# Optimization experiments

Hardware: AMD Instinct MI355X
Metric: run time of the kernel (lower is better)

## Reference

```python
import jax, jax.numpy as jnp
import numpy as np

B, N, H = 512, 100, 768
I = 2 * H  # intermediate_dim default = hidden_dim * 2
NUM_ANS = 16
MAX_ANS = 15
LN_EPS = 1e-5


def setup_inputs() -> dict:
    key = jax.random.key(0)
    ks = jax.random.split(key, 7)
    s = 0.02
    return {
        "v_emb": jax.random.normal(ks[0], (B, N, H), dtype=jnp.float32),
        "W1": jax.random.normal(ks[1], (H, I), dtype=jnp.float32) * s,
        "b1": jax.random.normal(ks[2], (I,), dtype=jnp.float32) * s,
        "gamma": jnp.ones((I,), dtype=jnp.float32),
        "beta": jnp.zeros((I,), dtype=jnp.float32),
        "W2": jax.random.normal(ks[3], (I, 1), dtype=jnp.float32) * s,
        "b2": jax.random.normal(ks[4], (1,), dtype=jnp.float32) * s,
    }


def reference(v_emb, W1, b1, gamma, beta, W2, b2):
    # Linear -> GELU (exact/erf, torch nn.GELU default) -> LayerNorm -> Linear
    h = jnp.einsum("bnh,hi->bni", v_emb, W1) + b1            # [B,N,I]
    h = jax.nn.gelu(h, approximate=False)
    mu = jnp.mean(h, axis=-1, keepdims=True)
    var = jnp.mean(jnp.square(h - mu), axis=-1, keepdims=True)
    h = (h - mu) * jax.lax.rsqrt(var + LN_EPS) * gamma + beta
    scores = jnp.einsum("bni,io->bno", h, W2) + b2           # [B,N,1]
    scores = jax.nn.sigmoid(scores)                           # sigmoid=True branch
    pred = jnp.sum(scores, axis=1)                            # [B,1]
    # pred_to_logits: vectorized round + clamp + one-hot scatter
    # str(int(round(p))) in {'0'..'15'} -> that id; negative -> 0; overflow -> max_ans
    aid = jnp.clip(jnp.round(pred[:, 0]).astype(jnp.int32), 0, MAX_ANS)
    logits = jax.nn.one_hot(aid, NUM_ANS, dtype=scores.dtype)  # [B,16]
    # original returns dict: scores, final_attention_map (==scores), pred, logits
    return scores, pred, logits
```

## Files before the change

### kernel.cpp

```cpp
#include <hip/hip_runtime.h>
#include <hip/hip_bf16.h>
#include <cstdint>
#include <cstddef>

#define BB   512
#define NN   100
#define HH   768
#define II   1536
#define MM   (BB*NN)

typedef __bf16 bf16;
typedef __bf16 bf16x4 __attribute__((ext_vector_type(4)));
typedef __bf16 bf16x8 __attribute__((ext_vector_type(8)));
typedef float  f32x4  __attribute__((ext_vector_type(4)));

__device__ __forceinline__ void gld_lds16(const bf16* g, bf16* l) {
    __builtin_amdgcn_global_load_lds(
        (const __attribute__((address_space(1))) void*)g,
        (__attribute__((address_space(3))) void*)l, 16, 0, 0);
}

template <int PAT>
__device__ __forceinline__ float swz_add(float x) {
    return x + __int_as_float(
        __builtin_amdgcn_ds_swizzle(__float_as_int(x), PAT));
}
__device__ __forceinline__ float red16(float x) {
    x = swz_add<0x041F>(x);
    x = swz_add<0x081F>(x);
    x = swz_add<0x101F>(x);
    x = swz_add<0x201F>(x);
    return x;
}

__device__ __forceinline__ float fast_gelu(float x) {
    const float ax = fabsf(x) * 0.70710678118654752f;
    const float t  = __builtin_amdgcn_rcpf(fmaf(0.3275911f, ax, 1.0f));
    float p = fmaf(1.061405429f, t, -1.453152027f);
    p = fmaf(p, t, 1.421413741f);
    p = fmaf(p, t, -0.284496736f);
    p = fmaf(p, t, 0.254829592f);
    p = p * t;
    const float e    = __expf(-ax * ax);
    const float erfa = fmaf(-p, e, 1.0f);
    const float erfx = copysignf(erfa, x);
    return 0.5f * x * (1.0f + erfx);
}

__global__ __launch_bounds__(256) void prep_kernel(
    const float* __restrict__ W1, const float* __restrict__ gamma,
    const float* __restrict__ beta, const float* __restrict__ W2,
    const float* __restrict__ b2,
    bf16* __restrict__ Wp, float* __restrict__ gw, float* __restrict__ scal)
{
    int bid = blockIdx.x;
    if (bid < 1152) {
        int t  = bid * 256 + threadIdx.x;
        int n  = t % II;
        int k0 = (t / II) * 4;
        bf16x4 v;
        v[0] = (bf16)W1[(size_t)(k0+0)*II + n];
        v[1] = (bf16)W1[(size_t)(k0+1)*II + n];
        v[2] = (bf16)W1[(size_t)(k0+2)*II + n];
        v[3] = (bf16)W1[(size_t)(k0+3)*II + n];
        *(bf16x4*)&Wp[(size_t)n*HH + k0] = v;
    } else if (bid == 1152) {
        for (int j = threadIdx.x; j < II; j += 256)
            gw[j] = gamma[j] * W2[j];
    } else {
        float s1 = 0.f, s2 = 0.f;
        for (int j = threadIdx.x; j < II; j += 256) {
            float w2 = W2[j];
            s1 += gamma[j] * w2;
            s2 += beta[j]  * w2;
        }
        #pragma unroll
        for (int off = 32; off; off >>= 1) {
            s1 += __shfl_down(s1, off, 64);
            s2 += __shfl_down(s2, off, 64);
        }
        __shared__ float a1[4], a2[4];
        int lane = threadIdx.x & 63, w = threadIdx.x >> 6;
        if (lane == 0) { a1[w] = s1; a2[w] = s2; }
        __syncthreads();
        if (threadIdx.x == 0) {
            scal[0] = a1[0] + a1[1] + a1[2] + a1[3];
            scal[1] = a2[0] + a2[1] + a2[2] + a2[3] + b2[0];
        }
    }
}

__global__ __launch_bounds__(256) void gemm_part(
    const float* __restrict__ Af, const bf16* __restrict__ Wp,
    const float* __restrict__ b1, const float* __restrict__ gw,
    float* __restrict__ part)
{
    __shared__ bf16  As[128 * 64];
    __shared__ bf16  Bs[128 * 64];
    __shared__ float sred[2][128][3];

    const int tid  = threadIdx.x;
    const int lin  = (blockIdx.x % 8) * 600 + blockIdx.x / 8;
    const int mb   = lin / 12;
    const int nb   = lin % 12;
    const int lane = tid & 63;
    const int w    = tid >> 6;
    const int wm   = w >> 1;
    const int wn   = w & 1;
    const int m15  = lane & 15;
    const int q    = lane >> 4;
    const int row0 = mb * 128;

    const int rsub = tid >> 3;
    const int kg   = (tid & 7) ^ (rsub & 7);
    const int lbase = tid * 8;

    const float* aP = Af + (size_t)(row0    + rsub) * HH + kg * 8;
    const bf16*  bP = Wp + (size_t)(nb*128 + rsub) * HH + kg * 8;

    f32x4 acc[4][4] = {};

    for (int kt = 0; kt < 12; ++kt) {
        #pragma unroll
        for (int it = 0; it < 4; ++it)
            gld_lds16(bP + (size_t)it * 32 * HH, &Bs[lbase + it * 2048]);
        #pragma unroll
        for (int it = 0; it < 4; ++it) {
            const float* s = aP + (size_t)it * 32 * HH;
            float4 v0 = *(const float4*)(s);
            float4 v1 = *(const float4*)(s + 4);
            bf16x8 o = { (bf16)v0.x, (bf16)v0.y, (bf16)v0.z, (bf16)v0.w,
                         (bf16)v1.x, (bf16)v1.y, (bf16)v1.z, (bf16)v1.w };
            *(bf16x8*)&As[lbase + it * 2048] = o;
        }
        asm volatile("s_waitcnt vmcnt(0)" ::: "memory");
        __syncthreads();

        #pragma unroll
        for (int kb = 0; kb < 2; ++kb) {
            const int swz = (((kb * 4 + q) ^ (m15 & 7)) * 8);
            bf16x8 af[4], bfr[4];
            #pragma unroll
            for (int mt = 0; mt < 4; ++mt)
                af[mt] = *(const bf16x8*)&As[(wm*64 + mt*16 + m15) * 64 + swz];
            #pragma unroll
            for (int nt = 0; nt < 4; ++nt)
                bfr[nt] = *(const bf16x8*)&Bs[(wn*64 + nt*16 + m15) * 64 + swz];
            #pragma unroll
            for (int mt = 0; mt < 4; ++mt)
                #pragma unroll
                for (int nt = 0; nt < 4; ++nt)
                    acc[mt][nt] = __builtin_amdgcn_mfma_f32_16x16x32_bf16(
                        af[mt], bfr[nt], acc[mt][nt], 0, 0, 0);
        }
        __syncthreads();
        aP += 64; bP += 64;
    }

    float bv[4], gv[4];
    #pragma unroll
    for (int nt = 0; nt < 4; ++nt) {
        const int col = nb*128 + wn*64 + nt*16 + m15;
        bv[nt] = b1[col];
        gv[nt] = gw[col];
    }

    #pragma unroll
    for (int mt = 0; mt < 4; ++mt) {
        #pragma unroll
        for (int r = 0; r < 4; ++r) {
            float x0 = 0.f, x1 = 0.f, x2 = 0.f;
            #pragma unroll
            for (int nt = 0; nt < 4; ++nt) {
                float g = fast_gelu(acc[mt][nt][r] + bv[nt]);
                x0 += g; x1 += g * g; x2 += g * gv[nt];
            }
            x0 = red16(x0); x1 = red16(x1); x2 = red16(x2);
            if (m15 == 0) {
                const int rl = wm*64 + mt*16 + q*4 + r;
                sred[wn][rl][0] = x0;
                sred[wn][rl][1] = x1;
                sred[wn][rl][2] = x2;
            }
        }
    }
    __syncthreads();

    if (tid < 128) {
        const size_t rg = (size_t)row0 + tid;
        #pragma unroll
        for (int s = 0; s < 3; ++s)
            part[(size_t)s * 12 * MM + (size_t)nb * MM + rg]
                = sred[0][tid][s] + sred[1][tid][s];
    }
}

__global__ __launch_bounds__(128) void score_pred(
    const float* __restrict__ part, const float* __restrict__ scal,
    float* __restrict__ o_scores, float* __restrict__ o_pred,
    float* __restrict__ o_logits)
{
    const int b = blockIdx.x, t = threadIdx.x;
    float s = 0.f;
    if (t < NN) {
        const size_t row = (size_t)b * NN + t;
        float Sh = 0.f, Shh = 0.f, Shg = 0.f;
        #pragma unroll
        for (int j = 0; j < 12; ++j) {
            Sh  += part[(size_t)0*12*MM + (size_t)j*MM + row];
            Shh += part[(size_t)1*12*MM + (size_t)j*MM + row];
            Shg += part[(size_t)2*12*MM + (size_t)j*MM + row];
        }
        const float mu   = Sh * (1.0f / II);
        const float var  = Shh * (1.0f / II) - mu * mu;
        const float rstd = rsqrtf(var + 1e-5f);
        const float z    = rstd * (Shg - mu * scal[0]) + scal[1];
        s = 1.0f / (1.0f + __expf(-z));
        o_scores[row] = s;
    }
    float v = s;
    #pragma unroll
    for (int off = 32; off; off >>= 1) v += __shfl_down(v, off, 64);
    __shared__ float ssum[2];
    const int lane = t & 63, w = t >> 6;
    if (lane == 0) ssum[w] = v;
    __syncthreads();
    const float p = ssum[0] + ssum[1];
    if (t == 0) o_pred[b] = p;
    if (t < 16) {
        int aid = (int)rintf(p);
        aid = aid < 0 ? 0 : (aid > 15 ? 15 : aid);
        o_logits[b * 16 + t] = (t == aid) ? 1.0f : 0.0f;
    }
}

extern "C" void kernel_launch(void* const* d_in, const int* in_sizes, int n_in,
                              void* d_out, int out_size, void* d_ws, size_t ws_size,
                              hipStream_t stream)
{
    const float* v_emb = (const float*)d_in[0];
    const float* W1    = (const float*)d_in[1];
    const float* b1    = (const float*)d_in[2];
    const float* gamma = (const float*)d_in[3];
    const float* beta  = (const float*)d_in[4];
    const float* W2    = (const float*)d_in[5];
    const float* b2    = (const float*)d_in[6];

    char* ws = (char*)d_ws;
    size_t off = 0;
    bf16*  Wp   = (bf16*)(ws + off);  off += (size_t)II * HH * 2;
    float* gw   = (float*)(ws + off); off += (size_t)II * 4;
    float* scal = (float*)(ws + off); off += 256;
    float* part = (float*)(ws + off); off += (size_t)MM * 36 * 4;

    float* out       = (float*)d_out;
    float* o_scores  = out;
    float* o_pred    = out + MM;
    float* o_logits  = out + MM + BB;

    hipLaunchKernelGGL(prep_kernel, dim3(1154), dim3(256), 0, stream,
                       W1, gamma, beta, W2, b2, Wp, gw, scal);
    hipLaunchKernelGGL(gemm_part, dim3((MM / 128) * 12), dim3(256),
                       0, stream, v_emb, Wp, b1, gw, part);
    hipLaunchKernelGGL(score_pred, dim3(BB), dim3(128), 0, stream,
                       part, scal, o_scores, o_pred, o_logits);
}
```

Baseline: 394.0 us.

## Load fp32 A tiles directly to LDS and tile-transpose W1 in prep

```diff
diff --git a/kernel.cpp b/kernel.cpp
--- a/kernel.cpp
+++ b/kernel.cpp
@@ -14,7 +14,7 @@
 typedef __bf16 bf16x8 __attribute__((ext_vector_type(8)));
 typedef float  f32x4  __attribute__((ext_vector_type(4)));
 
-__device__ __forceinline__ void gld_lds16(const bf16* g, bf16* l) {
+__device__ __forceinline__ void gld_lds16(const void* g, void* l) {
     __builtin_amdgcn_global_load_lds(
         (const __attribute__((address_space(1))) void*)g,
         (__attribute__((address_space(3))) void*)l, 16, 0, 0);
@@ -53,23 +53,37 @@
     const float* __restrict__ b2,
     bf16* __restrict__ Wp, float* __restrict__ gw, float* __restrict__ scal)
 {
-    int bid = blockIdx.x;
-    if (bid < 1152) {
-        int t  = bid * 256 + threadIdx.x;
-        int n  = t % II;
-        int k0 = (t / II) * 4;
-        bf16x4 v;
-        v[0] = (bf16)W1[(size_t)(k0+0)*II + n];
-        v[1] = (bf16)W1[(size_t)(k0+1)*II + n];
-        v[2] = (bf16)W1[(size_t)(k0+2)*II + n];
-        v[3] = (bf16)W1[(size_t)(k0+3)*II + n];
-        *(bf16x4*)&Wp[(size_t)n*HH + k0] = v;
-    } else if (bid == 1152) {
-        for (int j = threadIdx.x; j < II; j += 256)
+    const int bid = blockIdx.x, tid = threadIdx.x;
+    if (bid < 288) {
+        __shared__ bf16 Ts[64 * 72];
+        const int kt = bid % 12, nt = bid / 12;
+        const int k0 = kt * 64, n0 = nt * 64;
+        #pragma unroll
+        for (int it = 0; it < 4; ++it) {
+            const int idx = it * 256 + tid;
+            const int r   = idx >> 4;
+            const int c4  = idx & 15;
+            float4 v = *(const float4*)&W1[(size_t)(k0 + r) * II + n0 + c4*4];
+            Ts[(c4*4 + 0) * 72 + r] = (bf16)v.x;
+            Ts[(c4*4 + 1) * 72 + r] = (bf16)v.y;
+            Ts[(c4*4 + 2) * 72 + r] = (bf16)v.z;
+            Ts[(c4*4 + 3) * 72 + r] = (bf16)v.w;
+        }
+        __syncthreads();
+        #pragma unroll
+        for (int it = 0; it < 2; ++it) {
+            const int idx = it * 256 + tid;
+            const int nr  = idx >> 3;
+            const int kc  = idx & 7;
+            *(bf16x8*)&Wp[(size_t)(n0 + nr) * HH + k0 + kc*8]
+                = *(const bf16x8*)&Ts[nr * 72 + kc*8];
+        }
+    } else if (bid == 288) {
+        for (int j = tid; j < II; j += 256)
             gw[j] = gamma[j] * W2[j];
     } else {
         float s1 = 0.f, s2 = 0.f;
-        for (int j = threadIdx.x; j < II; j += 256) {
+        for (int j = tid; j < II; j += 256) {
             float w2 = W2[j];
             s1 += gamma[j] * w2;
             s2 += beta[j]  * w2;
@@ -80,10 +94,10 @@
             s2 += __shfl_down(s2, off, 64);
         }
         __shared__ float a1[4], a2[4];
-        int lane = threadIdx.x & 63, w = threadIdx.x >> 6;
+        int lane = tid & 63, w = tid >> 6;
         if (lane == 0) { a1[w] = s1; a2[w] = s2; }
         __syncthreads();
-        if (threadIdx.x == 0) {
+        if (tid == 0) {
             scal[0] = a1[0] + a1[1] + a1[2] + a1[3];
             scal[1] = a2[0] + a2[1] + a2[2] + a2[3] + b2[0];
         }
@@ -95,9 +109,8 @@
     const float* __restrict__ b1, const float* __restrict__ gw,
     float* __restrict__ part)
 {
-    __shared__ bf16  As[128 * 64];
+    __shared__ float AsF[128 * 64];
     __shared__ bf16  Bs[128 * 64];
-    __shared__ float sred[2][128][3];
 
     const int tid  = threadIdx.x;
     const int lin  = (blockIdx.x % 8) * 600 + blockIdx.x / 8;
@@ -111,38 +124,43 @@
     const int q    = lane >> 4;
     const int row0 = mb * 128;
 
-    const int rsub = tid >> 3;
-    const int kg   = (tid & 7) ^ (rsub & 7);
-    const int lbase = tid * 8;
-
-    const float* aP = Af + (size_t)(row0    + rsub) * HH + kg * 8;
-    const bf16*  bP = Wp + (size_t)(nb*128 + rsub) * HH + kg * 8;
+    const int ar = tid >> 4;
+    const int h  = tid & 15;
+    const int ap = h >> 1;
+    const int asl = ap ^ (ar & 7);
+    const float* aP = Af + (size_t)(row0 + ar) * HH + asl * 8 + (h & 1) * 4;
+
+    const int br = tid >> 3;
+    const int bsl = (tid & 7) ^ (br & 7);
+    const bf16* bP = Wp + (size_t)(nb*128 + br) * HH + bsl * 8;
 
     f32x4 acc[4][4] = {};
 
     for (int kt = 0; kt < 12; ++kt) {
         #pragma unroll
         for (int it = 0; it < 4; ++it)
-            gld_lds16(bP + (size_t)it * 32 * HH, &Bs[lbase + it * 2048]);
-        #pragma unroll
-        for (int it = 0; it < 4; ++it) {
-            const float* s = aP + (size_t)it * 32 * HH;
-            float4 v0 = *(const float4*)(s);
-            float4 v1 = *(const float4*)(s + 4);
-            bf16x8 o = { (bf16)v0.x, (bf16)v0.y, (bf16)v0.z, (bf16)v0.w,
-                         (bf16)v1.x, (bf16)v1.y, (bf16)v1.z, (bf16)v1.w };
-            *(bf16x8*)&As[lbase + it * 2048] = o;
-        }
+            gld_lds16(bP + (size_t)it * 32 * HH, &Bs[tid*8 + it*2048]);
+        #pragma unroll
+        for (int it = 0; it < 8; ++it)
+            gld_lds16(aP + (size_t)it * 16 * HH, &AsF[tid*4 + it*1024]);
         asm volatile("s_waitcnt vmcnt(0)" ::: "memory");
         __syncthreads();
 
         #pragma unroll
         for (int kb = 0; kb < 2; ++kb) {
-            const int swz = (((kb * 4 + q) ^ (m15 & 7)) * 8);
+            const int pk_ = kb * 4 + q;
             bf16x8 af[4], bfr[4];
             #pragma unroll
-            for (int mt = 0; mt < 4; ++mt)
-                af[mt] = *(const bf16x8*)&As[(wm*64 + mt*16 + m15) * 64 + swz];
+            for (int mt = 0; mt < 4; ++mt) {
+                const int rr = wm*64 + mt*16 + m15;
+                const int fb = rr * 64 + (pk_ ^ (rr & 7)) * 8;
+                f32x4 lo = *(const f32x4*)&AsF[fb];
+                f32x4 hi = *(const f32x4*)&AsF[fb + 4];
+                af[mt] = bf16x8{ (bf16)lo[0], (bf16)lo[1], (bf16)lo[2],
+                                 (bf16)lo[3], (bf16)hi[0], (bf16)hi[1],
+                                 (bf16)hi[2], (bf16)hi[3] };
+            }
+            const int swz = (pk_ ^ (m15 & 7)) * 8;
             #pragma unroll
             for (int nt = 0; nt < 4; ++nt)
                 bfr[nt] = *(const bf16x8*)&Bs[(wn*64 + nt*16 + m15) * 64 + swz];
@@ -156,6 +174,8 @@
         __syncthreads();
         aP += 64; bP += 64;
     }
+
+    float* sred = (float*)Bs;
 
     float bv[4], gv[4];
     #pragma unroll
@@ -178,9 +198,9 @@
             x0 = red16(x0); x1 = red16(x1); x2 = red16(x2);
             if (m15 == 0) {
                 const int rl = wm*64 + mt*16 + q*4 + r;
-                sred[wn][rl][0] = x0;
-                sred[wn][rl][1] = x1;
-                sred[wn][rl][2] = x2;
+                sred[wn*384 + rl*3 + 0] = x0;
+                sred[wn*384 + rl*3 + 1] = x1;
+                sred[wn*384 + rl*3 + 2] = x2;
             }
         }
     }
@@ -191,7 +211,7 @@
         #pragma unroll
         for (int s = 0; s < 3; ++s)
             part[(size_t)s * 12 * MM + (size_t)nb * MM + rg]
-                = sred[0][tid][s] + sred[1][tid][s];
+                = sred[0*384 + tid*3 + s] + sred[1*384 + tid*3 + s];
     }
 }
 
@@ -258,7 +278,7 @@
     float* o_pred    = out + MM;
     float* o_logits  = out + MM + BB;
 
-    hipLaunchKernelGGL(prep_kernel, dim3(1154), dim3(256), 0, stream,
+    hipLaunchKernelGGL(prep_kernel, dim3(290), dim3(256), 0, stream,
                        W1, gamma, beta, W2, b2, Wp, gw, scal);
     hipLaunchKernelGGL(gemm_part, dim3((MM / 128) * 12), dim3(256),
                        0, stream, v_emb, Wp, b1, gw, part);
```

New measurement: 459.5 us. +16.6%, slower.
